# Performance work log

Measured on AMD Instinct MI355X. Metric: run time of the kernel, lower is better.

## Reference

```python
import jax, jax.numpy as jnp
import numpy as np

WIDTH = 256
HEAD = 16
SCALE = 2
G = WIDTH // HEAD          # 16 groups
NH = G * SCALE             # 32 kernelized heads
EPS = 1e-5
N_NODES = 20000
B_GRAPHS = 1024


def setup_inputs() -> dict:
    key = jax.random.key(0)
    ks = jax.random.split(key, 10)
    x = jax.random.normal(ks[0], (N_NODES, WIDTH), jnp.float32)
    x_res = jax.random.normal(ks[1], (B_GRAPHS, NH, HEAD, HEAD), jnp.float32)
    batch = jnp.sort(jax.random.randint(ks[2], (N_NODES,), 0, B_GRAPHS)).astype(jnp.int64)
    w_pre = jax.random.normal(ks[3], (WIDTH, WIDTH), jnp.float32) * 0.02
    b_pre = jnp.zeros((WIDTH,), jnp.float32)
    # grouped 1x1 convs: [groups, width_scale, head_out, head_in]
    wq = jax.random.normal(ks[4], (G, SCALE, HEAD, HEAD), jnp.float32) * 0.02
    wk = jax.random.normal(ks[5], (G, SCALE, HEAD, HEAD), jnp.float32) * 0.02
    wv = jax.random.normal(ks[6], (G, SCALE, HEAD, HEAD), jnp.float32) * 0.02
    w_post = jax.random.normal(ks[7], (WIDTH, WIDTH * SCALE), jnp.float32) * 0.02
    b_post = jnp.zeros((WIDTH,), jnp.float32)
    log_scale = jnp.full((WIDTH,), np.log(0.01), jnp.float32)
    return {"x": x, "x_res": x_res, "batch": batch, "batch_size": B_GRAPHS,
            "w_pre": w_pre, "b_pre": b_pre, "wq": wq, "wk": wk, "wv": wv,
            "w_post": w_post, "b_post": b_post, "log_scale": log_scale}


def reference(x, x_res, batch, batch_size, w_pre, b_pre, wq, wk, wv, w_post, b_post, log_scale):
    n = x.shape[0]
    # pre: 1x1 conv (= linear) + GroupNorm(affine=False); L=1 so normalize over
    # each group's width_head channels.
    y = x @ w_pre.T + b_pre                       # [N, width]
    yg = y.reshape(n, G, HEAD)                    # [N, G, Hd]
    mu = yg.mean(-1, keepdims=True)
    var = yg.var(-1, keepdims=True)               # biased, as in GroupNorm
    yn = (yg - mu) / jnp.sqrt(var + EPS)          # [N, G, Hd]

    inv_sqrt_h = 1.0 / np.sqrt(HEAD)
    # grouped convs -> kernelized q,k (exp) and v
    xq = jnp.exp(jnp.einsum('ngi,gsoi->ngso', yn, wq) * inv_sqrt_h).reshape(n, NH, HEAD)
    xk = jnp.exp(jnp.einsum('ngi,gsoi->ngso', yn, wk) * inv_sqrt_h).reshape(n, NH, HEAD)
    xv = jnp.einsum('ngi,gsoi->ngso', yn, wv).reshape(n, NH, HEAD)

    # outer product k (x) v then scatter-sum over graphs  [B, NH, Hd, Hd]
    kv = jnp.einsum('bnh,bnv->bnhv', xk, xv)
    kv_sum = jax.ops.segment_sum(kv, batch, num_segments=batch_size) + x_res
    x_res_out = kv_sum

    # per-graph key sum, gathered back to nodes
    k_sum = jax.ops.segment_sum(xk, batch, num_segments=batch_size)[batch]  # [N, NH, Hd]
    denom = jnp.einsum('bnh,bnh->bn', xq, k_sum)                            # [N, NH]
    qn = xq / denom[:, :, None]

    out = jnp.einsum('bnh,bnhv->bnv', qn, kv_sum[batch]).reshape(n, WIDTH * SCALE)
    out = jnp.exp(log_scale) * (out @ w_post.T + b_post)                    # [N, width]
    return (out, x_res_out)
```

## Files before the change

kernel.cpp:

```cpp
#include <hip/hip_runtime.h>
#include <stdint.h>

typedef unsigned int u32;
typedef unsigned short u16;
typedef __attribute__((ext_vector_type(8))) short v8s;
typedef __attribute__((ext_vector_type(4))) float v4f;

#define GN_EPS 1e-5f

__device__ __forceinline__ float bflo(u32 u){ return __uint_as_float(u << 16); }
__device__ __forceinline__ float bfhi(u32 u){ return __uint_as_float(u & 0xffff0000u); }
__device__ __forceinline__ u16 f2bf(float f){
  u32 x = __float_as_uint(f);
  u32 r = (x + 0x7fffu + ((x >> 16) & 1u)) >> 16;
  return (u16)r;
}
__device__ __forceinline__ u32 pack2(float a, float b){
  return (u32)f2bf(a) | ((u32)f2bf(b) << 16);
}
__device__ __forceinline__ void unpack8(const uint4 u, float* f){
  f[0]=bflo(u.x); f[1]=bfhi(u.x); f[2]=bflo(u.y); f[3]=bfhi(u.y);
  f[4]=bflo(u.z); f[5]=bfhi(u.z); f[6]=bflo(u.w); f[7]=bfhi(u.w);
}
__device__ __forceinline__ uint4 loadpack8(const float* __restrict__ p){
  float4 a = *(const float4*)p, b = *(const float4*)(p + 4);
  return make_uint4(pack2(a.x,a.y),pack2(a.z,a.w),pack2(b.x,b.y),pack2(b.z,b.w));
}

__device__ __forceinline__ int getb(const int* __restrict__ b, int is64, int i){
  return b[is64 ? 2*i : i];
}

__global__ __launch_bounds__(256) void k_detect(
    const int* __restrict__ batch, int n, int* __restrict__ flags)
{
  int i = blockIdx.x*256 + threadIdx.x;
  int bad = 0;
  if (i < n - 1 && batch[i] > batch[i + 1]) bad = 1;
  if (__builtin_amdgcn_ballot_w64(bad) != 0 && (threadIdx.x & 63) == 0)
    atomicOr(&flags[0], 1);
}

__global__ __launch_bounds__(256) void k_bounds(
    const int* __restrict__ batch, const int* __restrict__ flags,
    int N, int B, int* __restrict__ bounds)
{
  int i = blockIdx.x*256 + threadIdx.x;
  if (i >= N) return;
  const int is64 = flags[0];
  int b = getb(batch, is64, i);
  int prev = (i == 0) ? -1 : getb(batch, is64, i - 1);
  for (int g = prev + 1; g <= b; g++) bounds[g] = i;
  if (i == N - 1)
    for (int g = b + 1; g <= B; g++) bounds[g] = N;
}

__global__ __launch_bounds__(256) void k_pre(
    const float* __restrict__ x, const float* __restrict__ wpre,
    const float* __restrict__ bpre, float* __restrict__ y, int N, int nbm)
{
  __shared__ __align__(16) u16 As[128*40];
  __shared__ __align__(16) u16 Bs[64*40];
  const int t = threadIdx.x;
  const int bm = blockIdx.x % nbm;
  const int bn = blockIdx.x / nbm;
  const int m_base = bm*128, n_base = bn*64;
  const int w = t >> 6, lane = t & 63;
  const int wr = (w >> 1)*64, wc = (w & 1)*32;
  const int fr = lane & 15, fk = lane >> 4;
  const int arow = t >> 1, acol = (t & 1)*16;
  const int brow = t >> 2, bcol = (t & 3)*8;

  v4f acc[4][2];
#pragma unroll
  for (int i = 0; i < 4; i++)
#pragma unroll
    for (int j = 0; j < 2; j++) acc[i][j] = (v4f){0.f,0.f,0.f,0.f};

  for (int k0 = 0; k0 < 256; k0 += 32) {
    __syncthreads();
    {
      int gm = m_base + arow;
      uint4 a0 = make_uint4(0u,0u,0u,0u), a1 = make_uint4(0u,0u,0u,0u);
      if (gm < N) {
        a0 = loadpack8(x + (size_t)gm*256 + k0 + acol);
        a1 = loadpack8(x + (size_t)gm*256 + k0 + acol + 8);
      }
      *(uint4*)&As[arow*40 + acol]     = a0;
      *(uint4*)&As[arow*40 + acol + 8] = a1;
      uint4 bv = loadpack8(wpre + (size_t)(n_base + brow)*256 + k0 + bcol);
      *(uint4*)&Bs[brow*40 + bcol] = bv;
    }
    __syncthreads();
    v8s b0 = *(const v8s*)&Bs[(wc      + fr)*40 + fk*8];
    v8s b1 = *(const v8s*)&Bs[(wc + 16 + fr)*40 + fk*8];
#pragma unroll
    for (int mi = 0; mi < 4; mi++) {
      v8s a = *(const v8s*)&As[(wr + mi*16 + fr)*40 + fk*8];
      acc[mi][0] = __builtin_amdgcn_mfma_f32_16x16x32_bf16(a,b0,acc[mi][0],0,0,0);
      acc[mi][1] = __builtin_amdgcn_mfma_f32_16x16x32_bf16(a,b1,acc[mi][1],0,0,0);
    }
  }
#pragma unroll
  for (int nj = 0; nj < 2; nj++) {
    int col = n_base + wc + nj*16 + fr;
    float bpv = bpre[col];
#pragma unroll
    for (int mi = 0; mi < 4; mi++) {
#pragma unroll
      for (int r = 0; r < 4; r++) {
        int row = m_base + wr + mi*16 + fk*4 + r;
        if (row < N) y[(size_t)row*256 + col] = acc[mi][nj][r] + bpv;
      }
    }
  }
}

__global__ __launch_bounds__(256) void k_gnqkv(
    const float* __restrict__ y, const float* __restrict__ wq,
    const float* __restrict__ wk, const float* __restrict__ wv,
    u16* __restrict__ qo, u16* __restrict__ ko, u16* __restrict__ vo, int N)
{
  __shared__ __align__(16) float wL[3*512];
  const int t = threadIdx.x;
  const int g = blockIdx.x & 15;
  const int c = blockIdx.x >> 4;
  {
    const float* srcs[3] = {wq, wk, wv};
#pragma unroll
    for (int tz = 0; tz < 3; tz++) {
      wL[tz*512 + t]       = srcs[tz][g*512 + t];
      wL[tz*512 + t + 256] = srcs[tz][g*512 + t + 256];
    }
  }
  __syncthreads();
  const int node = c*256 + t;
  if (node >= N) return;

  const float* yp = y + (size_t)node*256 + g*16;
  float4 v0 = *(const float4*)yp;
  float4 v1 = *(const float4*)(yp + 4);
  float4 v2 = *(const float4*)(yp + 8);
  float4 v3 = *(const float4*)(yp + 12);
  float a[16] = {v0.x,v0.y,v0.z,v0.w, v1.x,v1.y,v1.z,v1.w,
                 v2.x,v2.y,v2.z,v2.w, v3.x,v3.y,v3.z,v3.w};
  float mu = 0.f;
#pragma unroll
  for (int i = 0; i < 16; i++) mu += a[i];
  mu *= 0.0625f;
  float s2 = 0.f;
#pragma unroll
  for (int i = 0; i < 16; i++) { float d = a[i]-mu; s2 = fmaf(d,d,s2); }
  float inv = rsqrtf(s2*0.0625f + GN_EPS);
  float yn[16];
#pragma unroll
  for (int i = 0; i < 16; i++) yn[i] = (a[i]-mu)*inv;

  u16* outs[3] = {qo, ko, vo};
#pragma unroll
  for (int tz = 0; tz < 3; tz++) {
#pragma unroll
    for (int s = 0; s < 2; s++) {
      u32 p[8];
#pragma unroll
      for (int o = 0; o < 16; o++) {
        const float* row = &wL[tz*512 + (s*16 + o)*16];
        float4 W0 = *(const float4*)row;
        float4 W1 = *(const float4*)(row + 4);
        float4 W2 = *(const float4*)(row + 8);
        float4 W3 = *(const float4*)(row + 12);
        float w[16] = {W0.x,W0.y,W0.z,W0.w,W1.x,W1.y,W1.z,W1.w,
                       W2.x,W2.y,W2.z,W2.w,W3.x,W3.y,W3.z,W3.w};
        float d = 0.f;
#pragma unroll
        for (int i = 0; i < 16; i++) d = fmaf(yn[i], w[i], d);
        if (tz < 2) d = __expf(d*0.25f);
        if (o & 1) p[o>>1] |= (u32)f2bf(d) << 16;
        else       p[o>>1]  = (u32)f2bf(d);
      }
      u16* dst = outs[tz] + (size_t)node*512 + g*32 + s*16;
      *(uint4*)dst       = make_uint4(p[0],p[1],p[2],p[3]);
      *(uint4*)(dst + 8) = make_uint4(p[4],p[5],p[6],p[7]);
    }
  }
}

__global__ __launch_bounds__(512) void k_segatt(
    const u16* __restrict__ xk, const u16* __restrict__ xv,
    const u16* __restrict__ xq, const float* __restrict__ xres,
    const int* __restrict__ bounds,
    float* __restrict__ out1, u16* __restrict__ att, int N)
{
  __shared__ __align__(16) float red[512*20];
  __shared__ __align__(16) float kspart[512];
  __shared__ __align__(16) u16 kvs[32*280];
  __shared__ float kss[32*17];
  const int b = blockIdx.x, t = threadIdx.x;
  const int lo = bounds[b], hi = bounds[b+1];
  const int half = t >> 8;
  const int nh = (t >> 3) & 31, hp = t & 7;

  float kv[2][16];
#pragma unroll
  for (int r = 0; r < 2; r++)
#pragma unroll
    for (int v = 0; v < 16; v++) kv[r][v] = 0.f;
  float ks0 = 0.f, ks1 = 0.f;

  const size_t koff = (size_t)nh*16 + 2*hp;
  const size_t voff = (size_t)nh*16;
  int node = lo + half;
  for (; node + 2 < hi; node += 4) {
    u32  kw0 = *(const u32*) (xk + (size_t)node*512 + koff);
    uint4 Va0 = *(const uint4*)(xv + (size_t)node*512 + voff);
    uint4 Va1 = *(const uint4*)(xv + (size_t)node*512 + voff + 8);
    u32  kw1 = *(const u32*) (xk + (size_t)(node+2)*512 + koff);
    uint4 Vb0 = *(const uint4*)(xv + (size_t)(node+2)*512 + voff);
    uint4 Vb1 = *(const uint4*)(xv + (size_t)(node+2)*512 + voff + 8);
    float a0 = bflo(kw0), a1 = bfhi(kw0);
    float b0 = bflo(kw1), b1 = bfhi(kw1);
    float va[16], vb[16];
    unpack8(Va0, va); unpack8(Va1, va + 8);
    unpack8(Vb0, vb); unpack8(Vb1, vb + 8);
    ks0 += a0 + b0; ks1 += a1 + b1;
#pragma unroll
    for (int v = 0; v < 16; v++) {
      kv[0][v] = fmaf(a0, va[v], kv[0][v]);
      kv[1][v] = fmaf(a1, va[v], kv[1][v]);
      kv[0][v] = fmaf(b0, vb[v], kv[0][v]);
      kv[1][v] = fmaf(b1, vb[v], kv[1][v]);
    }
  }
  if (node < hi) {
    u32  kw = *(const u32*) (xk + (size_t)node*512 + koff);
    uint4 V0 = *(const uint4*)(xv + (size_t)node*512 + voff);
    uint4 V1 = *(const uint4*)(xv + (size_t)node*512 + voff + 8);
    float k0 = bflo(kw), k1 = bfhi(kw);
    float vf[16]; unpack8(V0, vf); unpack8(V1, vf + 8);
    ks0 += k0; ks1 += k1;
#pragma unroll
    for (int v = 0; v < 16; v++) {
      kv[0][v] = fmaf(k0, vf[v], kv[0][v]);
      kv[1][v] = fmaf(k1, vf[v], kv[1][v]);
    }
  }

  if (half == 0) {
#pragma unroll
    for (int r = 0; r < 2; r++) {
      float* rp = &red[(nh*16 + 2*hp + r)*20];
      *(float4*)rp       = make_float4(kv[r][0], kv[r][1], kv[r][2], kv[r][3]);
      *(float4*)(rp + 4) = make_float4(kv[r][4], kv[r][5], kv[r][6], kv[r][7]);
      *(float4*)(rp + 8) = make_float4(kv[r][8], kv[r][9], kv[r][10],kv[r][11]);
      *(float4*)(rp + 12)= make_float4(kv[r][12],kv[r][13],kv[r][14],kv[r][15]);
    }
    kspart[nh*16 + 2*hp]     = ks0;
    kspart[nh*16 + 2*hp + 1] = ks1;
  }
  __syncthreads();

  if (half == 1) {
#pragma unroll
    for (int r = 0; r < 2; r++) {
      const float* rp = &red[(nh*16 + 2*hp + r)*20];
      float4 R0 = *(const float4*)rp;
      float4 R1 = *(const float4*)(rp + 4);
      float4 R2 = *(const float4*)(rp + 8);
      float4 R3 = *(const float4*)(rp + 12);
      kv[r][0] += R0.x; kv[r][1] += R0.y; kv[r][2] += R0.z; kv[r][3] += R0.w;
      kv[r][4] += R1.x; kv[r][5] += R1.y; kv[r][6] += R1.z; kv[r][7] += R1.w;
      kv[r][8] += R2.x; kv[r][9] += R2.y; kv[r][10]+= R2.z; kv[r][11]+= R2.w;
      kv[r][12]+= R3.x; kv[r][13]+= R3.y; kv[r][14]+= R3.z; kv[r][15]+= R3.w;
    }
    ks0 += kspart[nh*16 + 2*hp];
    ks1 += kspart[nh*16 + 2*hp + 1];
    kss[nh*17 + 2*hp]     = ks0;
    kss[nh*17 + 2*hp + 1] = ks1;

#pragma unroll
    for (int r = 0; r < 2; r++) {
      int h = 2*hp + r;
      size_t idx = ((size_t)(b*32 + nh)*16 + h)*16;
      const float* xp = xres + idx;
      float4 X0 = *(const float4*)xp;
      float4 X1 = *(const float4*)(xp + 4);
      float4 X2 = *(const float4*)(xp + 8);
      float4 X3 = *(const float4*)(xp + 12);
      float xf[16] = {X0.x,X0.y,X0.z,X0.w,X1.x,X1.y,X1.z,X1.w,
                      X2.x,X2.y,X2.z,X2.w,X3.x,X3.y,X3.z,X3.w};
      float o[16];
#pragma unroll
      for (int j = 0; j < 16; j++) o[j] = kv[r][j] + xf[j];
      float* op = out1 + idx;
      *(float4*)op        = make_float4(o[0],o[1],o[2],o[3]);
      *(float4*)(op + 4)  = make_float4(o[4],o[5],o[6],o[7]);
      *(float4*)(op + 8)  = make_float4(o[8],o[9],o[10],o[11]);
      *(float4*)(op + 12) = make_float4(o[12],o[13],o[14],o[15]);
      u16* lp = &kvs[nh*280 + h*16];
      *(uint4*)lp       = make_uint4(pack2(o[0],o[1]),  pack2(o[2],o[3]),
                                     pack2(o[4],o[5]),  pack2(o[6],o[7]));
      *(uint4*)(lp + 8) = make_uint4(pack2(o[8],o[9]),  pack2(o[10],o[11]),
                                     pack2(o[12],o[13]),pack2(o[14],o[15]));
    }
  }
  __syncthreads();

  const int nh2 = t & 31, ns = t >> 5;
  for (int n0 = lo; n0 < hi; n0 += 16) {
    int nodei = n0 + ns;
    if (nodei >= hi) continue;
    const u16* qp = xq + (size_t)nodei*512 + nh2*16;
    uint4 Q0 = *(const uint4*)qp;
    uint4 Q1 = *(const uint4*)(qp + 8);
    float q[16]; unpack8(Q0, q); unpack8(Q1, q + 8);
    const float* ksp = &kss[nh2*17];
    float denom = 0.f;
#pragma unroll
    for (int i = 0; i < 16; i++) denom = fmaf(q[i], ksp[i], denom);
    float inv = 1.0f / fmaxf(denom, 1e-20f);
    float a[16];
#pragma unroll
    for (int v = 0; v < 16; v++) a[v] = 0.f;
    const u16* kvp = &kvs[nh2*280];
#pragma unroll
    for (int h = 0; h < 16; h++) {
      float qh = q[h] * inv;
      uint4 W0 = *(const uint4*)(kvp + h*16);
      uint4 W1 = *(const uint4*)(kvp + h*16 + 8);
      float w[16]; unpack8(W0, w); unpack8(W1, w + 8);
#pragma unroll
      for (int v = 0; v < 16; v++) a[v] = fmaf(qh, w[v], a[v]);
    }
    u32 p[8];
#pragma unroll
    for (int j = 0; j < 8; j++) p[j] = pack2(a[2*j], a[2*j+1]);
    u16* dst = att + (size_t)nodei*512 + nh2*16;
    *(uint4*)dst       = make_uint4(p[0],p[1],p[2],p[3]);
    *(uint4*)(dst + 8) = make_uint4(p[4],p[5],p[6],p[7]);
  }
}

__global__ __launch_bounds__(256) void k_post(
    const u16* __restrict__ att, const float* __restrict__ wpost,
    const float* __restrict__ bpost, const float* __restrict__ ls,
    float* __restrict__ out0, int N, int nbm)
{
  __shared__ __align__(16) u16 As[128*40];
  __shared__ __align__(16) u16 Bs[64*40];
  const int t = threadIdx.x;
  const int bm = blockIdx.x % nbm;
  const int bn = blockIdx.x / nbm;
  const int m_base = bm*128, n_base = bn*64;
  const int w = t >> 6, lane = t & 63;
  const int wr = (w >> 1)*64, wc = (w & 1)*32;
  const int fr = lane & 15, fk = lane >> 4;
  const int arow = t >> 1, acol = (t & 1)*16;
  const int brow = t >> 2, bcol = (t & 3)*8;

  v4f acc[4][2];
#pragma unroll
  for (int i = 0; i < 4; i++)
#pragma unroll
    for (int j = 0; j < 2; j++) acc[i][j] = (v4f){0.f,0.f,0.f,0.f};

  for (int k0 = 0; k0 < 512; k0 += 32) {
    __syncthreads();
    {
      int gm = m_base + arow;
      uint4 a0 = make_uint4(0u,0u,0u,0u), a1 = make_uint4(0u,0u,0u,0u);
      if (gm < N) {
        a0 = *(const uint4*)(att + (size_t)gm*512 + k0 + acol);
        a1 = *(const uint4*)(att + (size_t)gm*512 + k0 + acol + 8);
      }
      *(uint4*)&As[arow*40 + acol]     = a0;
      *(uint4*)&As[arow*40 + acol + 8] = a1;
      uint4 bv = loadpack8(wpost + (size_t)(n_base + brow)*512 + k0 + bcol);
      *(uint4*)&Bs[brow*40 + bcol] = bv;
    }
    __syncthreads();
    v8s b0 = *(const v8s*)&Bs[(wc      + fr)*40 + fk*8];
    v8s b1 = *(const v8s*)&Bs[(wc + 16 + fr)*40 + fk*8];
#pragma unroll
    for (int mi = 0; mi < 4; mi++) {
      v8s a = *(const v8s*)&As[(wr + mi*16 + fr)*40 + fk*8];
      acc[mi][0] = __builtin_amdgcn_mfma_f32_16x16x32_bf16(a,b0,acc[mi][0],0,0,0);
      acc[mi][1] = __builtin_amdgcn_mfma_f32_16x16x32_bf16(a,b1,acc[mi][1],0,0,0);
    }
  }
#pragma unroll
  for (int nj = 0; nj < 2; nj++) {
    int col = n_base + wc + nj*16 + fr;
    float bpv = bpost[col];
    float e   = __expf(ls[col]);
#pragma unroll
    for (int mi = 0; mi < 4; mi++) {
#pragma unroll
      for (int r = 0; r < 4; r++) {
        int row = m_base + wr + mi*16 + fk*4 + r;
        if (row < N) out0[(size_t)row*256 + col] = e*(acc[mi][nj][r] + bpv);
      }
    }
  }
}

extern "C" void kernel_launch(void* const* d_in, const int* in_sizes, int n_in,
                              void* d_out, int out_size, void* d_ws, size_t ws_size,
                              hipStream_t stream)
{
  const float* x     = (const float*)d_in[0];
  const float* xres  = (const float*)d_in[1];
  const int*   batch = (const int*)d_in[2];
  const float* wpre  = (const float*)d_in[4];
  const float* bpre  = (const float*)d_in[5];
  const float* wq    = (const float*)d_in[6];
  const float* wk    = (const float*)d_in[7];
  const float* wv    = (const float*)d_in[8];
  const float* wpost = (const float*)d_in[9];
  const float* bpost = (const float*)d_in[10];
  const float* ls    = (const float*)d_in[11];

  const int N = in_sizes[0] / 256;
  const int B = in_sizes[1] / 8192;
  const int nbm = (N + 127) / 128;
  const int nchunk = (N + 255) / 256;

  char* ws = (char*)d_ws;
  size_t off = 0;
  int*   flags  = (int*)(ws + off); off += 256;
  int*   bounds = (int*)(ws + off); off += ((size_t)B + 64) * 4;
  float* y      = (float*)(ws + off);
  u16*   att    = (u16*)(ws + off);  off += (size_t)N * 1024;
  u16*   q      = (u16*)(ws + off);  off += (size_t)N * 1024;
  u16*   kten   = (u16*)(ws + off);  off += (size_t)N * 1024;
  u16*   vten   = (u16*)(ws + off);  off += (size_t)N * 1024;

  float* out0 = (float*)d_out;
  float* out1 = out0 + (size_t)N * 256;

  hipMemsetAsync(flags, 0, 4, stream);
  k_detect<<<nchunk,         256, 0, stream>>>(batch, N, flags);
  k_bounds<<<nchunk,         256, 0, stream>>>(batch, flags, N, B, bounds);
  k_pre   <<<nbm * 4,        256, 0, stream>>>(x, wpre, bpre, y, N, nbm);
  k_gnqkv <<<nchunk * 16,    256, 0, stream>>>(y, wq, wk, wv, q, kten, vten, N);
  k_segatt<<<B,              512, 0, stream>>>(kten, vten, q, xres, bounds,
                                               out1, att, N);
  k_post  <<<nbm * 4,        256, 0, stream>>>(att, wpost, bpost, ls, out0, N, nbm);
}
```

Baseline: 136.9 us.

## Store K/V transposed and compute per-graph KV sums with MFMA

k_gnqkv now writes K and V in a head-dim-major transposed layout (padded length Npad) so that a graph's nodes are contiguous per feature row. k_segatt replaces the scalar per-thread outer-product accumulation and LDS cross-half reduction with bf16 MFMA 16x16x32 over 32-node chunks. Out-of-segment nodes are masked to zero, and the key sum is obtained by an MFMA against a masked ones vector. This trades scattered 2-byte transposed stores in k_gnqkv, plus reads of padding and neighbouring-graph nodes, for far fewer VALU FMAs in the segment reduction.

```diff
diff --git a/kernel.cpp b/kernel.cpp
--- a/kernel.cpp
+++ b/kernel.cpp
@@ -7,6 +7,8 @@
 typedef __attribute__((ext_vector_type(4))) float v4f;
 
 #define GN_EPS 1e-5f
+
+union U4V8 { uint4 u; v8s s; };
 
 __device__ __forceinline__ float bflo(u32 u){ return __uint_as_float(u << 16); }
 __device__ __forceinline__ float bfhi(u32 u){ return __uint_as_float(u & 0xffff0000u); }
@@ -116,10 +118,29 @@
   }
 }
 
+__device__ __forceinline__ float dot16(const float* __restrict__ yn,
+                                       const float* __restrict__ row){
+  float4 W0 = *(const float4*)row;
+  float4 W1 = *(const float4*)(row + 4);
+  float4 W2 = *(const float4*)(row + 8);
+  float4 W3 = *(const float4*)(row + 12);
+  float d = 0.f;
+  d = fmaf(yn[0],W0.x,d); d = fmaf(yn[1],W0.y,d);
+  d = fmaf(yn[2],W0.z,d); d = fmaf(yn[3],W0.w,d);
+  d = fmaf(yn[4],W1.x,d); d = fmaf(yn[5],W1.y,d);
+  d = fmaf(yn[6],W1.z,d); d = fmaf(yn[7],W1.w,d);
+  d = fmaf(yn[8],W2.x,d); d = fmaf(yn[9],W2.y,d);
+  d = fmaf(yn[10],W2.z,d); d = fmaf(yn[11],W2.w,d);
+  d = fmaf(yn[12],W3.x,d); d = fmaf(yn[13],W3.y,d);
+  d = fmaf(yn[14],W3.z,d); d = fmaf(yn[15],W3.w,d);
+  return d;
+}
+
 __global__ __launch_bounds__(256) void k_gnqkv(
     const float* __restrict__ y, const float* __restrict__ wq,
     const float* __restrict__ wk, const float* __restrict__ wv,
-    u16* __restrict__ qo, u16* __restrict__ ko, u16* __restrict__ vo, int N)
+    u16* __restrict__ qo, u16* __restrict__ kT, u16* __restrict__ vT,
+    int N, int Npad)
 {
   __shared__ __align__(16) float wL[3*512];
   const int t = threadIdx.x;
@@ -156,151 +177,100 @@
 #pragma unroll
   for (int i = 0; i < 16; i++) yn[i] = (a[i]-mu)*inv;
 
-  u16* outs[3] = {qo, ko, vo};
-#pragma unroll
-  for (int tz = 0; tz < 3; tz++) {
-#pragma unroll
-    for (int s = 0; s < 2; s++) {
-      u32 p[8];
-#pragma unroll
-      for (int o = 0; o < 16; o++) {
-        const float* row = &wL[tz*512 + (s*16 + o)*16];
-        float4 W0 = *(const float4*)row;
-        float4 W1 = *(const float4*)(row + 4);
-        float4 W2 = *(const float4*)(row + 8);
-        float4 W3 = *(const float4*)(row + 12);
-        float w[16] = {W0.x,W0.y,W0.z,W0.w,W1.x,W1.y,W1.z,W1.w,
-                       W2.x,W2.y,W2.z,W2.w,W3.x,W3.y,W3.z,W3.w};
-        float d = 0.f;
-#pragma unroll
-        for (int i = 0; i < 16; i++) d = fmaf(yn[i], w[i], d);
-        if (tz < 2) d = __expf(d*0.25f);
-        if (o & 1) p[o>>1] |= (u32)f2bf(d) << 16;
-        else       p[o>>1]  = (u32)f2bf(d);
-      }
-      u16* dst = outs[tz] + (size_t)node*512 + g*32 + s*16;
-      *(uint4*)dst       = make_uint4(p[0],p[1],p[2],p[3]);
-      *(uint4*)(dst + 8) = make_uint4(p[4],p[5],p[6],p[7]);
+#pragma unroll
+  for (int s = 0; s < 2; s++) {
+    u32 p[8];
+#pragma unroll
+    for (int o = 0; o < 16; o++) {
+      float d = __expf(dot16(yn, &wL[(s*16 + o)*16]) * 0.25f);
+      if (o & 1) p[o>>1] |= (u32)f2bf(d) << 16;
+      else       p[o>>1]  = (u32)f2bf(d);
+    }
+    u16* dst = qo + (size_t)node*512 + g*32 + s*16;
+    *(uint4*)dst       = make_uint4(p[0],p[1],p[2],p[3]);
+    *(uint4*)(dst + 8) = make_uint4(p[4],p[5],p[6],p[7]);
+  }
+#pragma unroll
+  for (int s = 0; s < 2; s++) {
+#pragma unroll
+    for (int o = 0; o < 16; o++) {
+      float d = __expf(dot16(yn, &wL[512 + (s*16 + o)*16]) * 0.25f);
+      kT[(size_t)((g*2 + s)*16 + o)*Npad + node] = f2bf(d);
+    }
+  }
+#pragma unroll
+  for (int s = 0; s < 2; s++) {
+#pragma unroll
+    for (int o = 0; o < 16; o++) {
+      float d = dot16(yn, &wL[1024 + (s*16 + o)*16]);
+      vT[(size_t)((g*2 + s)*16 + o)*Npad + node] = f2bf(d);
     }
   }
 }
 
 __global__ __launch_bounds__(512) void k_segatt(
-    const u16* __restrict__ xk, const u16* __restrict__ xv,
+    const u16* __restrict__ kT, const u16* __restrict__ vT,
     const u16* __restrict__ xq, const float* __restrict__ xres,
     const int* __restrict__ bounds,
-    float* __restrict__ out1, u16* __restrict__ att, int N)
-{
-  __shared__ __align__(16) float red[512*20];
-  __shared__ __align__(16) float kspart[512];
+    float* __restrict__ out1, u16* __restrict__ att, int N, int Npad)
+{
   __shared__ __align__(16) u16 kvs[32*280];
   __shared__ float kss[32*17];
   const int b = blockIdx.x, t = threadIdx.x;
   const int lo = bounds[b], hi = bounds[b+1];
-  const int half = t >> 8;
-  const int nh = (t >> 3) & 31, hp = t & 7;
-
-  float kv[2][16];
-#pragma unroll
-  for (int r = 0; r < 2; r++)
-#pragma unroll
-    for (int v = 0; v < 16; v++) kv[r][v] = 0.f;
-  float ks0 = 0.f, ks1 = 0.f;
-
-  const size_t koff = (size_t)nh*16 + 2*hp;
-  const size_t voff = (size_t)nh*16;
-  int node = lo + half;
-  for (; node + 2 < hi; node += 4) {
-    u32  kw0 = *(const u32*) (xk + (size_t)node*512 + koff);
-    uint4 Va0 = *(const uint4*)(xv + (size_t)node*512 + voff);
-    uint4 Va1 = *(const uint4*)(xv + (size_t)node*512 + voff + 8);
-    u32  kw1 = *(const u32*) (xk + (size_t)(node+2)*512 + koff);
-    uint4 Vb0 = *(const uint4*)(xv + (size_t)(node+2)*512 + voff);
-    uint4 Vb1 = *(const uint4*)(xv + (size_t)(node+2)*512 + voff + 8);
-    float a0 = bflo(kw0), a1 = bfhi(kw0);
-    float b0 = bflo(kw1), b1 = bfhi(kw1);
-    float va[16], vb[16];
-    unpack8(Va0, va); unpack8(Va1, va + 8);
-    unpack8(Vb0, vb); unpack8(Vb1, vb + 8);
-    ks0 += a0 + b0; ks1 += a1 + b1;
-#pragma unroll
-    for (int v = 0; v < 16; v++) {
-      kv[0][v] = fmaf(a0, va[v], kv[0][v]);
-      kv[1][v] = fmaf(a1, va[v], kv[1][v]);
-      kv[0][v] = fmaf(b0, vb[v], kv[0][v]);
-      kv[1][v] = fmaf(b1, vb[v], kv[1][v]);
-    }
-  }
-  if (node < hi) {
-    u32  kw = *(const u32*) (xk + (size_t)node*512 + koff);
-    uint4 V0 = *(const uint4*)(xv + (size_t)node*512 + voff);
-    uint4 V1 = *(const uint4*)(xv + (size_t)node*512 + voff + 8);
-    float k0 = bflo(kw), k1 = bfhi(kw);
-    float vf[16]; unpack8(V0, vf); unpack8(V1, vf + 8);
-    ks0 += k0; ks1 += k1;
-#pragma unroll
-    for (int v = 0; v < 16; v++) {
-      kv[0][v] = fmaf(k0, vf[v], kv[0][v]);
-      kv[1][v] = fmaf(k1, vf[v], kv[1][v]);
-    }
-  }
-
-  if (half == 0) {
-#pragma unroll
-    for (int r = 0; r < 2; r++) {
-      float* rp = &red[(nh*16 + 2*hp + r)*20];
-      *(float4*)rp       = make_float4(kv[r][0], kv[r][1], kv[r][2], kv[r][3]);
-      *(float4*)(rp + 4) = make_float4(kv[r][4], kv[r][5], kv[r][6], kv[r][7]);
-      *(float4*)(rp + 8) = make_float4(kv[r][8], kv[r][9], kv[r][10],kv[r][11]);
-      *(float4*)(rp + 12)= make_float4(kv[r][12],kv[r][13],kv[r][14],kv[r][15]);
-    }
-    kspart[nh*16 + 2*hp]     = ks0;
-    kspart[nh*16 + 2*hp + 1] = ks1;
-  }
-  __syncthreads();
-
-  if (half == 1) {
-#pragma unroll
-    for (int r = 0; r < 2; r++) {
-      const float* rp = &red[(nh*16 + 2*hp + r)*20];
-      float4 R0 = *(const float4*)rp;
-      float4 R1 = *(const float4*)(rp + 4);
-      float4 R2 = *(const float4*)(rp + 8);
-      float4 R3 = *(const float4*)(rp + 12);
-      kv[r][0] += R0.x; kv[r][1] += R0.y; kv[r][2] += R0.z; kv[r][3] += R0.w;
-      kv[r][4] += R1.x; kv[r][5] += R1.y; kv[r][6] += R1.z; kv[r][7] += R1.w;
-      kv[r][8] += R2.x; kv[r][9] += R2.y; kv[r][10]+= R2.z; kv[r][11]+= R2.w;
-      kv[r][12]+= R3.x; kv[r][13]+= R3.y; kv[r][14]+= R3.z; kv[r][15]+= R3.w;
-    }
-    ks0 += kspart[nh*16 + 2*hp];
-    ks1 += kspart[nh*16 + 2*hp + 1];
-    kss[nh*17 + 2*hp]     = ks0;
-    kss[nh*17 + 2*hp + 1] = ks1;
-
-#pragma unroll
-    for (int r = 0; r < 2; r++) {
-      int h = 2*hp + r;
-      size_t idx = ((size_t)(b*32 + nh)*16 + h)*16;
-      const float* xp = xres + idx;
-      float4 X0 = *(const float4*)xp;
-      float4 X1 = *(const float4*)(xp + 4);
-      float4 X2 = *(const float4*)(xp + 8);
-      float4 X3 = *(const float4*)(xp + 12);
-      float xf[16] = {X0.x,X0.y,X0.z,X0.w,X1.x,X1.y,X1.z,X1.w,
-                      X2.x,X2.y,X2.z,X2.w,X3.x,X3.y,X3.z,X3.w};
-      float o[16];
-#pragma unroll
-      for (int j = 0; j < 16; j++) o[j] = kv[r][j] + xf[j];
-      float* op = out1 + idx;
-      *(float4*)op        = make_float4(o[0],o[1],o[2],o[3]);
-      *(float4*)(op + 4)  = make_float4(o[4],o[5],o[6],o[7]);
-      *(float4*)(op + 8)  = make_float4(o[8],o[9],o[10],o[11]);
-      *(float4*)(op + 12) = make_float4(o[12],o[13],o[14],o[15]);
-      u16* lp = &kvs[nh*280 + h*16];
-      *(uint4*)lp       = make_uint4(pack2(o[0],o[1]),  pack2(o[2],o[3]),
-                                     pack2(o[4],o[5]),  pack2(o[6],o[7]));
-      *(uint4*)(lp + 8) = make_uint4(pack2(o[8],o[9]),  pack2(o[10],o[11]),
-                                     pack2(o[12],o[13]),pack2(o[14],o[15]));
+  const int w = t >> 6, lane = t & 63;
+  const int fr = lane & 15, fk = lane >> 4;
+
+  v4f akv[4], aks[4];
+#pragma unroll
+  for (int hh = 0; hh < 4; hh++) {
+    akv[hh] = (v4f){0.f,0.f,0.f,0.f};
+    aks[hh] = (v4f){0.f,0.f,0.f,0.f};
+  }
+
+  for (int n0 = (lo & ~31); n0 < hi; n0 += 32) {
+    const int nbase = n0 + fk*8;
+    u32 msk[4];
+#pragma unroll
+    for (int m = 0; m < 4; m++) {
+      int na = nbase + 2*m, nb = na + 1;
+      u32 mm = 0u;
+      if (na >= lo && na < hi) mm |= 0x0000FFFFu;
+      if (nb >= lo && nb < hi) mm |= 0xFFFF0000u;
+      msk[m] = mm;
+    }
+    U4V8 onesu;
+    onesu.u = make_uint4(msk[0] & 0x3F803F80u, msk[1] & 0x3F803F80u,
+                         msk[2] & 0x3F803F80u, msk[3] & 0x3F803F80u);
+#pragma unroll
+    for (int hh = 0; hh < 4; hh++) {
+      const int head = w*4 + hh;
+      U4V8 ku, vu;
+      ku.u = *(const uint4*)(kT + (size_t)(head*16 + fr)*Npad + nbase);
+      vu.u = *(const uint4*)(vT + (size_t)(head*16 + fr)*Npad + nbase);
+      ku.u.x &= msk[0]; ku.u.y &= msk[1]; ku.u.z &= msk[2]; ku.u.w &= msk[3];
+      vu.u.x &= msk[0]; vu.u.y &= msk[1]; vu.u.z &= msk[2]; vu.u.w &= msk[3];
+      akv[hh] = __builtin_amdgcn_mfma_f32_16x16x32_bf16(ku.s, vu.s, akv[hh],0,0,0);
+      aks[hh] = __builtin_amdgcn_mfma_f32_16x16x32_bf16(ku.s, onesu.s, aks[hh],0,0,0);
+    }
+  }
+
+#pragma unroll
+  for (int hh = 0; hh < 4; hh++) {
+    const int head = w*4 + hh;
+    const size_t hbase = ((size_t)b*32 + head)*256;
+#pragma unroll
+    for (int r = 0; r < 4; r++) {
+      int d = fk*4 + r;
+      size_t idx = hbase + d*16 + fr;
+      float o = akv[hh][r] + xres[idx];
+      out1[idx] = o;
+      kvs[head*280 + d*16 + fr] = f2bf(o);
+    }
+    if (fr == 0) {
+#pragma unroll
+      for (int r = 0; r < 4; r++)
+        kss[head*17 + fk*4 + r] = aks[hh][r];
     }
   }
   __syncthreads();
@@ -327,9 +297,9 @@
       float qh = q[h] * inv;
       uint4 W0 = *(const uint4*)(kvp + h*16);
       uint4 W1 = *(const uint4*)(kvp + h*16 + 8);
-      float w[16]; unpack8(W0, w); unpack8(W1, w + 8);
-#pragma unroll
-      for (int v = 0; v < 16; v++) a[v] = fmaf(qh, w[v], a[v]);
+      float wv[16]; unpack8(W0, wv); unpack8(W1, wv + 8);
+#pragma unroll
+      for (int v = 0; v < 16; v++) a[v] = fmaf(qh, wv[v], a[v]);
     }
     u32 p[8];
 #pragma unroll
@@ -423,6 +393,7 @@
   const int B = in_sizes[1] / 8192;
   const int nbm = (N + 127) / 128;
   const int nchunk = (N + 255) / 256;
+  const int Npad = ((N + 64 + 7) / 8) * 8;
 
   char* ws = (char*)d_ws;
   size_t off = 0;
@@ -431,8 +402,8 @@
   float* y      = (float*)(ws + off);
   u16*   att    = (u16*)(ws + off);  off += (size_t)N * 1024;
   u16*   q      = (u16*)(ws + off);  off += (size_t)N * 1024;
-  u16*   kten   = (u16*)(ws + off);  off += (size_t)N * 1024;
-  u16*   vten   = (u16*)(ws + off);  off += (size_t)N * 1024;
+  u16*   kT     = (u16*)(ws + off);  off += (size_t)512 * Npad * 2;
+  u16*   vT     = (u16*)(ws + off);  off += (size_t)512 * Npad * 2;
 
   float* out0 = (float*)d_out;
   float* out1 = out0 + (size_t)N * 256;
@@ -441,8 +412,8 @@
   k_detect<<<nchunk,         256, 0, stream>>>(batch, N, flags);
   k_bounds<<<nchunk,         256, 0, stream>>>(batch, flags, N, B, bounds);
   k_pre   <<<nbm * 4,        256, 0, stream>>>(x, wpre, bpre, y, N, nbm);
-  k_gnqkv <<<nchunk * 16,    256, 0, stream>>>(y, wq, wk, wv, q, kten, vten, N);
-  k_segatt<<<B,              512, 0, stream>>>(kten, vten, q, xres, bounds,
-                                               out1, att, N);
+  k_gnqkv <<<nchunk * 16,    256, 0, stream>>>(y, wq, wk, wv, q, kT, vT, N, Npad);
+  k_segatt<<<B,              512, 0, stream>>>(kT, vT, q, xres, bounds,
+                                               out1, att, N, Npad);
   k_post  <<<nbm * 4,        256, 0, stream>>>(att, wpost, bpost, ls, out0, N, nbm);
 }
```

New measurement: 136.2 us. About the same (-0.5%).
